# Optimization experiments

Hardware: AMD Instinct MI355X
Metric: run time of the kernel (lower is better)

The kernel has to match this reference:

```python
import jax, jax.numpy as jnp
import numpy as np

THETA0 = 3.0
THETA = 5.0
BIG = 1e10  # stands in for +inf in the squared-distance transform


def _edt_sq_1d(f):
    # f: [..., n] of squared distances; returns min_j (i-j)^2 + f[j] per i.
    n = f.shape[-1]
    i = jnp.arange(n, dtype=f.dtype)
    d2 = (i[:, None] - i[None, :]) ** 2  # [n, n]
    return jnp.min(f[..., None, :] + d2, axis=-1)


def _edt(mask):
    # Exact Euclidean distance from each voxel to the nearest zero of `mask`
    # (matches scipy.ndimage.distance_transform_edt on a binary mask),
    # via the separable squared-distance transform applied axis by axis.
    f = jnp.where(mask > 0.5, jnp.asarray(BIG, mask.dtype), jnp.asarray(0.0, mask.dtype))
    for ax in range(1, mask.ndim):  # skip batch axis 0
        f = jnp.moveaxis(_edt_sq_1d(jnp.moveaxis(f, ax, -1)), -1, ax)
    return jnp.sqrt(f)


def setup_inputs() -> dict:
    key = jax.random.key(0)
    k1, k2 = jax.random.split(key)
    B, D, H, W = 2, 64, 96, 96
    pred = jax.random.uniform(k1, (B, D, H, W), dtype=jnp.float32)  # probabilities
    target = jax.random.randint(k2, (B, D, H, W), 0, 2).astype(jnp.float32)  # binary mask
    return {"pred": pred, "target": target}


def reference(pred, target):
    # Signed distance phi = dist_to_foreground_boundary framework: 
    # dist_pos = EDT(target) (distance to nearest background voxel),
    # dist_neg = EDT(1 - target).
    dist_pos = _edt(target)
    dist_neg = _edt(1.0 - target)
    a = jnp.abs(dist_neg - dist_pos)
    w = jnp.where(
        a <= THETA0,
        1.0,
        jnp.where(a >= THETA, 0.0, 1.0 - (a - THETA0) / (THETA - THETA0)),
    )
    w = jax.lax.stop_gradient(w)  # original computes weights from detached numpy target

    # binary_cross_entropy with torch's log clamp at -100
    log_p = jnp.clip(jnp.log(pred), -100.0)
    log_1mp = jnp.clip(jnp.log(1.0 - pred), -100.0)
    bce = -(target * log_p + (1.0 - target) * log_1mp)  # [B, D, H, W]

    num = jnp.sum(bce * w, axis=(1, 2, 3))
    den = jnp.sum(w, axis=(1, 2, 3)) + 1e-5
    return jnp.mean(num / den)
```

## Files before the change

kernel.cpp:

```cpp
#include <hip/hip_runtime.h>
#include <math.h>

#define BDIM 2
#define DDIM 64
#define HDIM 96
#define WDIM 96
#define HW   (HDIM * WDIM)
#define DHW  (DDIM * HW)

#define DT 8
#define HT 8
#define WT 32
#define DH 16
#define HH 16
#define NROWS (DH * HH)
#define NBLK  (BDIM * (DDIM / DT) * (HDIM / HT) * (WDIM / WT))

__global__ void init_acc(float* __restrict__ acc) {
    if (threadIdx.x < 4) acc[threadIdx.x] = 0.0f;
    if (threadIdx.x == 4) ((int*)acc)[4] = 0;
}

__device__ __forceinline__ unsigned nearest2i(unsigned occ) {
    unsigned r = 25u;
    if (occ & 0x101u) r = 16u;
    if (occ & 0x082u) r = 9u;
    if (occ & 0x044u) r = 4u;
    if (occ & 0x028u) r = 1u;
    if (occ & 0x010u) r = 0u;
    return r;
}

__device__ __forceinline__ unsigned vminu4(unsigned a, unsigned b) {
    unsigned c = ((a | 0x80808080u) - b) & 0x80808080u;
    unsigned m = (c - (c >> 7)) | c;
    return a ^ ((a ^ b) & m);
}

__global__ __launch_bounds__(256) void boundary_fused(const float* __restrict__ pred,
                                                      const float* __restrict__ target,
                                                      float* __restrict__ acc,
                                                      float* __restrict__ out) {
    __shared__ unsigned long long fgb[NROWS];
    __shared__ unsigned swp[NROWS * 8];
    __shared__ unsigned swn[NROWS * 8];
    __shared__ unsigned whp[DH * HT * 8];
    __shared__ unsigned whn[DH * HT * 8];
    __shared__ float rsum[8];

    const int tid = threadIdx.x;
    int x = blockIdx.x;
    const int wt = x % 3;  x /= 3;
    const int ht = x % 12; x /= 12;
    const int dt = x % 8;
    const int b  = x / 8;
    const int d0 = dt * DT, h0 = ht * HT, w0 = wt * WT;

    unsigned long long vb_row = (1ULL << 40) - 1;
    if (wt == 0) vb_row &= ~0xFULL;
    if (wt == 2) vb_row &= (1ULL << 36) - 1;

    {
        const int lane = tid & 63;
        const int wv   = tid >> 6;
        #pragma unroll 4
        for (int i = 0; i < 64; ++i) {
            const int row = wv * 64 + i;
            const int dr = row >> 4, hr = row & 15;
            const int d = d0 - 4 + dr, h = h0 - 4 + hr, w = w0 - 4 + lane;
            const bool valid = (lane < 40) && ((unsigned)d < DDIM) &&
                               ((unsigned)h < HDIM) && ((unsigned)w < WDIM);
            float v = 0.0f;
            if (valid) v = target[((size_t)(b * DDIM + d) * HDIM + h) * WDIM + w];
            unsigned long long bb = __ballot(v > 0.5f);
            if (lane == 0) fgb[row] = bb;
        }
    }
    __syncthreads();

    {
        const int q  = tid & 7;
        const int rg = tid >> 3;
        #pragma unroll
        for (int k = 0; k < 8; ++k) {
            const int row = rg + 32 * k;
            const int dr = row >> 4, hr = row & 15;
            const bool rv = ((unsigned)(d0 - 4 + dr) < DDIM) &&
                            ((unsigned)(h0 - 4 + hr) < HDIM);
            const unsigned long long fg = fgb[row];
            const unsigned long long vb = rv ? vb_row : 0ULL;
            unsigned pa = 0u, na = 0u;
            #pragma unroll
            for (int j = 0; j < 4; ++j) {
                const int wi = q * 4 + j;
                const unsigned of = (unsigned)(fg >> wi) & 0x1FFu;
                const unsigned ov = (unsigned)(vb >> wi) & 0x1FFu;
                const unsigned ob = ~of & ov;
                na |= nearest2i(of) << (8 * j);
                pa |= nearest2i(ob) << (8 * j);
            }
            swp[row * 8 + q] = pa;
            swn[row * 8 + q] = na;
        }
    }
    __syncthreads();

    #pragma unroll
    for (int k = 0; k < 4; ++k) {
        const int g  = tid + 256 * k;
        const int q  = g & 7;
        const int hh = (g >> 3) & 7;
        const int dr = g >> 6;
        unsigned p = 0x19191919u, n = 0x19191919u;
        #pragma unroll
        for (int t = 0; t < 9; ++t) {
            const int dd = (t - 4) * (t - 4);
            const unsigned add = (unsigned)dd * 0x01010101u;
            const int src = (dr * HH + hh + t) * 8 + q;
            p = vminu4(p, swp[src] + add);
            n = vminu4(n, swn[src] + add);
        }
        whp[(dr * HT + hh) * 8 + q] = p;
        whn[(dr * HT + hh) * 8 + q] = n;
    }
    __syncthreads();

    float num = 0.f, den = 0.f;
    #pragma unroll
    for (int k = 0; k < 2; ++k) {
        const int g  = tid + 256 * k;
        const int q  = g & 7;
        const int hh = (g >> 3) & 7;
        const int di = g >> 6;
        unsigned p = 0x19191919u, n = 0x19191919u;
        #pragma unroll
        for (int t = 0; t < 9; ++t) {
            const int dd = (t - 4) * (t - 4);
            const unsigned add = (unsigned)dd * 0x01010101u;
            const int src = ((di + t) * HT + hh) * 8 + q;
            p = vminu4(p, whp[src] + add);
            n = vminu4(n, whn[src] + add);
        }
        const size_t gg = ((size_t)(b * DDIM + d0 + di) * HDIM + h0 + hh) * WDIM
                        + w0 + q * 4;
        const float4 pr = *(const float4*)(pred + gg);
        const float4 tg = *(const float4*)(target + gg);
        #pragma unroll
        for (int j = 0; j < 4; ++j) {
            const float pv = (float)((p >> (8 * j)) & 0xFFu);
            const float nv = (float)((n >> (8 * j)) & 0xFFu);
            const float prj = j == 0 ? pr.x : j == 1 ? pr.y : j == 2 ? pr.z : pr.w;
            const float tgj = j == 0 ? tg.x : j == 1 ? tg.y : j == 2 ? tg.z : tg.w;
            const float dp = sqrtf(pv);
            const float dn = sqrtf(nv);
            const float a  = fabsf(dn - dp);
            float w;
            if (a <= 3.0f)      w = 1.0f;
            else if (a >= 5.0f) w = 0.0f;
            else                w = 1.0f - (a - 3.0f) * 0.5f;
            const float lp  = fmaxf(logf(prj), -100.0f);
            const float l1  = fmaxf(logf(1.0f - prj), -100.0f);
            const float bce = -(tgj * lp + (1.0f - tgj) * l1);
            num += bce * w;
            den += w;
        }
    }

    for (int off = 32; off > 0; off >>= 1) {
        num += __shfl_down(num, off);
        den += __shfl_down(den, off);
    }
    if ((tid & 63) == 0) {
        rsum[tid >> 6]       = num;
        rsum[4 + (tid >> 6)] = den;
    }
    __syncthreads();
    if (tid == 0) {
        float ns = rsum[0] + rsum[1] + rsum[2] + rsum[3];
        float ds = rsum[4] + rsum[5] + rsum[6] + rsum[7];
        atomicAdd(&acc[b], ns);
        atomicAdd(&acc[2 + b], ds);
        __threadfence();
        int done = atomicAdd((int*)acc + 4, 1);
        if (done == NBLK - 1) {
            __threadfence();
            float n0  = atomicAdd(&acc[0], 0.0f);
            float n1  = atomicAdd(&acc[1], 0.0f);
            float d0_ = atomicAdd(&acc[2], 0.0f);
            float d1_ = atomicAdd(&acc[3], 0.0f);
            out[0] = 0.5f * (n0 / (d0_ + 1e-5f) + n1 / (d1_ + 1e-5f));
        }
    }
}

extern "C" void kernel_launch(void* const* d_in, const int* in_sizes, int n_in,
                              void* d_out, int out_size, void* d_ws, size_t ws_size,
                              hipStream_t stream) {
    const float* pred   = (const float*)d_in[0];
    const float* target = (const float*)d_in[1];
    float* acc = (float*)d_ws;
    float* out = (float*)d_out;

    init_acc<<<1, 64, 0, stream>>>(acc);
    boundary_fused<<<NBLK, 256, 0, stream>>>(pred, target, acc, out);
}
```

Measured before the change: 109.3 us.

## Load target halo as float4 into byte masks and compute W-pass with packed SWAR

The halo load now reads target as float4 instead of scalar per-lane ballots, and packs each group of four voxels into byte-wise foreground and background masks in shared memory. The W-axis nearest-distance pass is rebuilt as byte-parallel SWAR on those packed words (alignbyte shifts plus vector min) instead of per-voxel bit tests with branches. The H-pass output buffers reuse the mask arrays to keep LDS use down. This cuts global load instructions and ALU work in the first stages. The background mask is computed only for in-bounds words, so edge handling now relies on how the out-of-range words are treated.

```diff
diff --git a/kernel.cpp b/kernel.cpp
--- a/kernel.cpp
+++ b/kernel.cpp
@@ -5,8 +5,6 @@
 #define DDIM 64
 #define HDIM 96
 #define WDIM 96
-#define HW   (HDIM * WDIM)
-#define DHW  (DDIM * HW)
 
 #define DT 8
 #define HT 8
@@ -21,32 +19,44 @@
     if (threadIdx.x == 4) ((int*)acc)[4] = 0;
 }
 
-__device__ __forceinline__ unsigned nearest2i(unsigned occ) {
-    unsigned r = 25u;
-    if (occ & 0x101u) r = 16u;
-    if (occ & 0x082u) r = 9u;
-    if (occ & 0x044u) r = 4u;
-    if (occ & 0x028u) r = 1u;
-    if (occ & 0x010u) r = 0u;
-    return r;
-}
-
 __device__ __forceinline__ unsigned vminu4(unsigned a, unsigned b) {
     unsigned c = ((a | 0x80808080u) - b) & 0x80808080u;
     unsigned m = (c - (c >> 7)) | c;
     return a ^ ((a ^ b) & m);
 }
 
+__device__ __forceinline__ unsigned shiftw(unsigned lo, unsigned hi, int t) {
+#if __has_builtin(__builtin_amdgcn_alignbyte)
+    return __builtin_amdgcn_alignbyte(hi, lo, t);
+#else
+    return (lo >> (8 * t)) | (hi << (32 - 8 * t));
+#endif
+}
+
+__device__ __forceinline__ unsigned wpass_quad(unsigned W0, unsigned W1, unsigned W2) {
+    unsigned m = 0x19191919u - W1 * 25u;
+    unsigned u08 = W0 | W2;
+    m = vminu4(m, 0x19191919u - u08 * 9u);
+    unsigned u17 = shiftw(W0, W1, 1) | shiftw(W1, W2, 3);
+    m = vminu4(m, 0x19191919u - u17 * 16u);
+    unsigned u26 = shiftw(W0, W1, 2) | shiftw(W1, W2, 2);
+    m = vminu4(m, 0x19191919u - u26 * 21u);
+    unsigned u35 = shiftw(W0, W1, 3) | shiftw(W1, W2, 1);
+    m = vminu4(m, 0x19191919u - u35 * 24u);
+    return m;
+}
+
 __global__ __launch_bounds__(256) void boundary_fused(const float* __restrict__ pred,
                                                       const float* __restrict__ target,
                                                       float* __restrict__ acc,
                                                       float* __restrict__ out) {
-    __shared__ unsigned long long fgb[NROWS];
+    __shared__ unsigned fgm[NROWS * 10];
+    __shared__ unsigned bgm[NROWS * 10];
     __shared__ unsigned swp[NROWS * 8];
     __shared__ unsigned swn[NROWS * 8];
-    __shared__ unsigned whp[DH * HT * 8];
-    __shared__ unsigned whn[DH * HT * 8];
     __shared__ float rsum[8];
+    unsigned* whp = fgm;
+    unsigned* whn = bgm;
 
     const int tid = threadIdx.x;
     int x = blockIdx.x;
@@ -56,51 +66,36 @@
     const int b  = x / 8;
     const int d0 = dt * DT, h0 = ht * HT, w0 = wt * WT;
 
-    unsigned long long vb_row = (1ULL << 40) - 1;
-    if (wt == 0) vb_row &= ~0xFULL;
-    if (wt == 2) vb_row &= (1ULL << 36) - 1;
-
-    {
-        const int lane = tid & 63;
-        const int wv   = tid >> 6;
-        #pragma unroll 4
-        for (int i = 0; i < 64; ++i) {
-            const int row = wv * 64 + i;
-            const int dr = row >> 4, hr = row & 15;
-            const int d = d0 - 4 + dr, h = h0 - 4 + hr, w = w0 - 4 + lane;
-            const bool valid = (lane < 40) && ((unsigned)d < DDIM) &&
-                               ((unsigned)h < HDIM) && ((unsigned)w < WDIM);
-            float v = 0.0f;
-            if (valid) v = target[((size_t)(b * DDIM + d) * HDIM + h) * WDIM + w];
-            unsigned long long bb = __ballot(v > 0.5f);
-            if (lane == 0) fgb[row] = bb;
+    #pragma unroll
+    for (int k = 0; k < 10; ++k) {
+        const int idx = tid + 256 * k;
+        const int row = idx / 10;
+        const int q   = idx - row * 10;
+        const int dr = row >> 4, hr = row & 15;
+        const int d = d0 - 4 + dr, h = h0 - 4 + hr;
+        const int wb = w0 - 4 + 4 * q;
+        unsigned fgw = 0u, bgw = 0u;
+        if ((unsigned)d < DDIM && (unsigned)h < HDIM && (unsigned)wb < WDIM) {
+            const float4 v = *(const float4*)(target +
+                ((size_t)(b * DDIM + d) * HDIM + h) * WDIM + wb);
+            fgw = (unsigned)(v.x > 0.5f)        | ((unsigned)(v.y > 0.5f) << 8) |
+                  ((unsigned)(v.z > 0.5f) << 16) | ((unsigned)(v.w > 0.5f) << 24);
+            bgw = fgw ^ 0x01010101u;
         }
+        fgm[row * 10 + q] = fgw;
+        bgm[row * 10 + q] = bgw;
     }
     __syncthreads();
 
     {
-        const int q  = tid & 7;
-        const int rg = tid >> 3;
+        const int qp = tid & 7;
+        const int rb = tid >> 3;
         #pragma unroll
         for (int k = 0; k < 8; ++k) {
-            const int row = rg + 32 * k;
-            const int dr = row >> 4, hr = row & 15;
-            const bool rv = ((unsigned)(d0 - 4 + dr) < DDIM) &&
-                            ((unsigned)(h0 - 4 + hr) < HDIM);
-            const unsigned long long fg = fgb[row];
-            const unsigned long long vb = rv ? vb_row : 0ULL;
-            unsigned pa = 0u, na = 0u;
-            #pragma unroll
-            for (int j = 0; j < 4; ++j) {
-                const int wi = q * 4 + j;
-                const unsigned of = (unsigned)(fg >> wi) & 0x1FFu;
-                const unsigned ov = (unsigned)(vb >> wi) & 0x1FFu;
-                const unsigned ob = ~of & ov;
-                na |= nearest2i(of) << (8 * j);
-                pa |= nearest2i(ob) << (8 * j);
-            }
-            swp[row * 8 + q] = pa;
-            swn[row * 8 + q] = na;
+            const int row  = rb + 32 * k;
+            const int base = row * 10 + qp;
+            swn[row * 8 + qp] = wpass_quad(fgm[base], fgm[base + 1], fgm[base + 2]);
+            swp[row * 8 + qp] = wpass_quad(bgm[base], bgm[base + 1], bgm[base + 2]);
         }
     }
     __syncthreads();
@@ -114,8 +109,7 @@
         unsigned p = 0x19191919u, n = 0x19191919u;
         #pragma unroll
         for (int t = 0; t < 9; ++t) {
-            const int dd = (t - 4) * (t - 4);
-            const unsigned add = (unsigned)dd * 0x01010101u;
+            const unsigned add = (unsigned)((t - 4) * (t - 4)) * 0x01010101u;
             const int src = (dr * HH + hh + t) * 8 + q;
             p = vminu4(p, swp[src] + add);
             n = vminu4(n, swn[src] + add);
@@ -135,8 +129,7 @@
         unsigned p = 0x19191919u, n = 0x19191919u;
         #pragma unroll
         for (int t = 0; t < 9; ++t) {
-            const int dd = (t - 4) * (t - 4);
-            const unsigned add = (unsigned)dd * 0x01010101u;
+            const unsigned add = (unsigned)((t - 4) * (t - 4)) * 0x01010101u;
             const int src = ((di + t) * HT + hh) * 8 + q;
             p = vminu4(p, whp[src] + add);
             n = vminu4(n, whn[src] + add);
```

New measurement: 94.66 us. 13.4% less time.
